# Kernel tuning notes

Hardware: AMD Instinct MI355X
Metric: run time of the kernel (lower is better)

## Reference

```python
import jax, jax.numpy as jnp
import numpy as np

N, K, B, D, H = 256, 128, 256, 256, 512  # code length, info bits, batch, embed dim, MLP hidden


def _mlp(x, W1, b1, W2, b2):
    return jnp.maximum(x @ W1 + b1, 0.0) @ W2 + b2


def setup_inputs():
    key = jax.random.key(0)
    ks = jax.random.split(key, 12)
    perm = np.random.RandomState(0).permutation(N)
    info_set = jnp.sort(jnp.asarray(perm[:K], dtype=jnp.int32))  # unique sorted info positions
    info_bits = jax.random.randint(ks[0], (B, K), 0, 2, dtype=jnp.int32)
    rv = jax.random.uniform(ks[1], (B, N), dtype=jnp.float32)  # one uniform per leaf (sampling)

    def w(k, shape, fan):
        return jax.random.normal(k, shape, jnp.float32) / np.float32(np.sqrt(fan))

    return {
        'info_bits': info_bits,
        'rv': rv,
        'info_set': info_set,
        'obs_emb': w(ks[2], (3, D), D),
        'label_emb': w(ks[3], (3, D), D),
        'cn_W1': w(ks[4], (2 * D, H), 2 * D), 'cn_b1': jnp.zeros((H,), jnp.float32),
        'cn_W2': w(ks[5], (H, D), H), 'cn_b2': jnp.zeros((D,), jnp.float32),
        'bn_W1': w(ks[6], (3 * D, H), 3 * D), 'bn_b1': jnp.zeros((H,), jnp.float32),
        'bn_W2': w(ks[7], (H, D), H), 'bn_b2': jnp.zeros((D,), jnp.float32),
        'llr_W': w(ks[8], (D, 2), D), 'llr_b': jnp.zeros((2,), jnp.float32),
    }


def reference(info_bits, rv, info_set, obs_emb, label_emb,
              cn_W1, cn_b1, cn_W2, cn_b2, bn_W1, bn_b1, bn_W2, bn_b2, llr_W, llr_b):
    batch = info_bits.shape[0]

    def encode(e, f, off, n):
        # e: (B, n, D) float embeddings; f: (B, n, 1) int32 bits (2 == unknown -> sample)
        if n == 1:
            p_uy = jax.nn.softmax(e @ llr_W + llr_b, axis=-1)        # (B, 1, 2) probs
            r = rv[:, off:off + 1]                                    # (B, 1)
            # rv > cdf[...,0] == rv > p(u=0): sample a hard bit
            hard = (r > p_uy[..., 0]).astype(jnp.int32)[..., None]    # (B, 1, 1)
            x = jnp.where(f == 2, hard, f)
            return x, x, p_uy
        half = n // 2
        e_odd, e_even = e[:, ::2], e[:, 1::2]                         # SplitEvenOdd(axis=1)
        f_left, f_right = f[:, :half], f[:, half:]
        u1est = _mlp(jnp.concatenate([e_odd, e_even], -1), cn_W1, cn_b1, cn_W2, cn_b2)
        u1, h1, p_left = encode(u1est, f_left, off, half)
        u_emb = label_emb[h1[..., 0]]                                 # (B, half, D)
        u2est = _mlp(jnp.concatenate([e_odd, e_even, u_emb], -1), bn_W1, bn_b1, bn_W2, bn_b2)
        u2, h2, p_right = encode(u2est, f_right, off + half, half)
        u = jnp.concatenate([u1, u2], 1)
        p_uy = jnp.concatenate([p_left, p_right], 1)
        v_xor = jnp.mod(h1 + h2, 2)
        # Interleave(axis=1): out[::2] = v_xor, out[1::2] = h2
        x = jnp.stack([v_xor, h2], axis=2).reshape(batch, n, 1)
        return u, x, p_uy

    # scatter info bits into the length-N frame (frozen positions stay == 2)
    u_ = jnp.full((batch, N), 2, jnp.int32).at[:, info_set].set(info_bits)
    f = u_[..., None]
    # embedding_observations_nn(2 * ones): embedding of token '2' everywhere
    e = jnp.broadcast_to(obs_emb[2], (batch, N, D))
    u, x, p_u = encode(e, f, 0, N)
    # f: sampled frame with info positions re-masked to 2
    f_out = u[..., 0].at[:, info_set].set(2)[..., None]
    return x, f_out, u, p_u
```

## Files before the change

### kernel.cpp

```cpp
#include <hip/hip_runtime.h>
#include <math.h>

#define NB 256
#define NN 256
#define NK 128
#define ND 256
#define NH 512
#define NT 1024

#define OUT_X 0
#define OUT_F 65536
#define OUT_U 131072
#define OUT_P 196608

#define EPB   65280
#define SP6O  EPB
#define S1O   (SP6O + 1024)
#define S2O   (S1O + 512)
#define S3O   (S2O + 1024)
#define LOFFI (S3O + 2048)
#define BPB   (LOFFI + 256)

__host__ __device__ __forceinline__ int loff(int d) { return 256 - (1 << (9 - d)); }

template <int PC>
__device__ void g1ks(const float* __restrict__ Abuf, float* __restrict__ part,
                     const int tid, const float* __restrict__ W1) {
  const int q = tid >> 8;
  const int c0 = (tid & 255) << 1;
  const float* Wp = W1 + (size_t)(q * 128) * NH + c0;
  const float* Ar = Abuf + q * 128;
  float a0[PC], a1[PC];
#pragma unroll
  for (int r = 0; r < PC; ++r) { a0[r] = 0.f; a1[r] = 0.f; }
  float2 n0 = *(const float2*)Wp;
  float2 n1 = *(const float2*)(Wp + NH);
  float2 n2 = *(const float2*)(Wp + 2 * NH);
  float2 n3 = *(const float2*)(Wp + 3 * NH);
#pragma unroll 2
  for (int kc = 0; kc < 124; kc += 4) {
    const float2 w0 = n0, w1 = n1, w2 = n2, w3 = n3;
    const float* Wn = Wp + (size_t)(kc + 4) * NH;
    n0 = *(const float2*)Wn;
    n1 = *(const float2*)(Wn + NH);
    n2 = *(const float2*)(Wn + 2 * NH);
    n3 = *(const float2*)(Wn + 3 * NH);
#pragma unroll
    for (int r = 0; r < PC; ++r) {
      const float4 av = *(const float4*)(Ar + r * 512 + kc);
      a0[r] += av.x * w0.x + av.y * w1.x + av.z * w2.x + av.w * w3.x;
      a1[r] += av.x * w0.y + av.y * w1.y + av.z * w2.y + av.w * w3.y;
    }
  }
#pragma unroll
  for (int r = 0; r < PC; ++r) {
    const float4 av = *(const float4*)(Ar + r * 512 + 124);
    a0[r] += av.x * n0.x + av.y * n1.x + av.z * n2.x + av.w * n3.x;
    a1[r] += av.x * n0.y + av.y * n1.y + av.z * n2.y + av.w * n3.y;
  }
#pragma unroll
  for (int r = 0; r < PC; ++r)
    *(float2*)&part[(q * PC + r) * 512 + c0] = make_float2(a0[r], a1[r]);
}

template <int RT>
__device__ void g2ks(const float* __restrict__ hid, const int hidBase,
                     float* __restrict__ part, const int tid,
                     const float* __restrict__ W2) {
  const int q = tid >> 7;
  const int c0 = (tid & 127) << 1;
  const float* Wp = W2 + (size_t)(q * 64) * ND + c0;
  const float* Hr = hid + hidBase * 512 + q * 64;
  float a0[RT], a1[RT];
#pragma unroll
  for (int r = 0; r < RT; ++r) { a0[r] = 0.f; a1[r] = 0.f; }
  float2 n0 = *(const float2*)Wp;
  float2 n1 = *(const float2*)(Wp + ND);
  float2 n2 = *(const float2*)(Wp + 2 * ND);
  float2 n3 = *(const float2*)(Wp + 3 * ND);
#pragma unroll 2
  for (int kc = 0; kc < 60; kc += 4) {
    const float2 w0 = n0, w1 = n1, w2 = n2, w3 = n3;
    const float* Wn = Wp + (size_t)(kc + 4) * ND;
    n0 = *(const float2*)Wn;
    n1 = *(const float2*)(Wn + ND);
    n2 = *(const float2*)(Wn + 2 * ND);
    n3 = *(const float2*)(Wn + 3 * ND);
#pragma unroll
    for (int r = 0; r < RT; ++r) {
      const float4 av = *(const float4*)(Hr + r * 512 + kc);
      a0[r] += av.x * w0.x + av.y * w1.x + av.z * w2.x + av.w * w3.x;
      a1[r] += av.x * w0.y + av.y * w1.y + av.z * w2.y + av.w * w3.y;
    }
  }
#pragma unroll
  for (int r = 0; r < RT; ++r) {
    const float4 av = *(const float4*)(Hr + r * 512 + 60);
    a0[r] += av.x * n0.x + av.y * n1.x + av.z * n2.x + av.w * n3.x;
    a1[r] += av.x * n0.y + av.y * n1.y + av.z * n2.y + av.w * n3.y;
  }
#pragma unroll
  for (int r = 0; r < RT; ++r)
    *(float2*)&part[(q * RT + r) * 256 + c0] = make_float2(a0[r], a1[r]);
}

template <int PC>
__device__ void g1q(const float* __restrict__ Abuf, float* __restrict__ part,
                    const int tid, const float* __restrict__ W1) {
  const int q = tid >> 7;
  const int c0 = (tid & 127) << 2;
  const float* Wp = W1 + (size_t)(q * 64) * NH + c0;
  const float* Ar = Abuf + q * 64;
  float a0[PC], a1[PC], a2[PC], a3[PC];
#pragma unroll
  for (int r = 0; r < PC; ++r) { a0[r] = 0.f; a1[r] = 0.f; a2[r] = 0.f; a3[r] = 0.f; }
  float4 n0 = *(const float4*)Wp;
  float4 n1 = *(const float4*)(Wp + NH);
  float4 n2 = *(const float4*)(Wp + 2 * NH);
  float4 n3 = *(const float4*)(Wp + 3 * NH);
#pragma unroll 2
  for (int kc = 0; kc < 60; kc += 4) {
    const float4 w0 = n0, w1 = n1, w2 = n2, w3 = n3;
    const float* Wn = Wp + (size_t)(kc + 4) * NH;
    n0 = *(const float4*)Wn;
    n1 = *(const float4*)(Wn + NH);
    n2 = *(const float4*)(Wn + 2 * NH);
    n3 = *(const float4*)(Wn + 3 * NH);
#pragma unroll
    for (int r = 0; r < PC; ++r) {
      const float4 av = *(const float4*)(Ar + r * 512 + kc);
      a0[r] += av.x * w0.x + av.y * w1.x + av.z * w2.x + av.w * w3.x;
      a1[r] += av.x * w0.y + av.y * w1.y + av.z * w2.y + av.w * w3.y;
      a2[r] += av.x * w0.z + av.y * w1.z + av.z * w2.z + av.w * w3.z;
      a3[r] += av.x * w0.w + av.y * w1.w + av.z * w2.w + av.w * w3.w;
    }
  }
#pragma unroll
  for (int r = 0; r < PC; ++r) {
    const float4 av = *(const float4*)(Ar + r * 512 + 60);
    a0[r] += av.x * n0.x + av.y * n1.x + av.z * n2.x + av.w * n3.x;
    a1[r] += av.x * n0.y + av.y * n1.y + av.z * n2.y + av.w * n3.y;
    a2[r] += av.x * n0.z + av.y * n1.z + av.z * n2.z + av.w * n3.z;
    a3[r] += av.x * n0.w + av.y * n1.w + av.z * n2.w + av.w * n3.w;
  }
#pragma unroll
  for (int r = 0; r < PC; ++r)
    *(float4*)&part[(q * PC + r) * 512 + c0] = make_float4(a0[r], a1[r], a2[r], a3[r]);
}

template <int RT>
__device__ void g2q(const float* __restrict__ hid, const int hidBase,
                    float* __restrict__ part, const int tid,
                    const float* __restrict__ W2) {
  const int q = tid >> 6;
  const int c0 = (tid & 63) << 2;
  const float* Wp = W2 + (size_t)(q * 32) * ND + c0;
  const float* Hr = hid + hidBase * 512 + q * 32;
  float a0[RT], a1[RT], a2[RT], a3[RT];
#pragma unroll
  for (int r = 0; r < RT; ++r) { a0[r] = 0.f; a1[r] = 0.f; a2[r] = 0.f; a3[r] = 0.f; }
  float4 n0 = *(const float4*)Wp;
  float4 n1 = *(const float4*)(Wp + ND);
  float4 n2 = *(const float4*)(Wp + 2 * ND);
  float4 n3 = *(const float4*)(Wp + 3 * ND);
#pragma unroll 2
  for (int kc = 0; kc < 28; kc += 4) {
    const float4 w0 = n0, w1 = n1, w2 = n2, w3 = n3;
    const float* Wn = Wp + (size_t)(kc + 4) * ND;
    n0 = *(const float4*)Wn;
    n1 = *(const float4*)(Wn + ND);
    n2 = *(const float4*)(Wn + 2 * ND);
    n3 = *(const float4*)(Wn + 3 * ND);
#pragma unroll
    for (int r = 0; r < RT; ++r) {
      const float4 av = *(const float4*)(Hr + r * 512 + kc);
      a0[r] += av.x * w0.x + av.y * w1.x + av.z * w2.x + av.w * w3.x;
      a1[r] += av.x * w0.y + av.y * w1.y + av.z * w2.y + av.w * w3.y;
      a2[r] += av.x * w0.z + av.y * w1.z + av.z * w2.z + av.w * w3.z;
      a3[r] += av.x * w0.w + av.y * w1.w + av.z * w2.w + av.w * w3.w;
    }
  }
#pragma unroll
  for (int r = 0; r < RT; ++r) {
    const float4 av = *(const float4*)(Hr + r * 512 + 28);
    a0[r] += av.x * n0.x + av.y * n1.x + av.z * n2.x + av.w * n3.x;
    a1[r] += av.x * n0.y + av.y * n1.y + av.z * n2.y + av.w * n3.y;
    a2[r] += av.x * n0.z + av.y * n1.z + av.z * n2.z + av.w * n3.z;
    a3[r] += av.x * n0.w + av.y * n1.w + av.z * n2.w + av.w * n3.w;
  }
#pragma unroll
  for (int r = 0; r < RT; ++r)
    *(float4*)&part[(q * RT + r) * 256 + c0] = make_float4(a0[r], a1[r], a2[r], a3[r]);
}

template <int KS, int PC>
__device__ void g1red(const float* __restrict__ part, float* __restrict__ hid,
                      const int tid, const float* __restrict__ b1,
                      const int isBn, const float* __restrict__ embS,
                      const int* __restrict__ bitR) {
  for (int i = tid; i < PC * 256; i += NT) {
    const int r = i >> 8, c0 = (i & 255) << 1;
    float2 s = *(const float2*)(b1 + c0);
#pragma unroll
    for (int qq = 0; qq < KS; ++qq) {
      const float2 p = *(const float2*)&part[(qq * PC + r) * 512 + c0];
      s.x += p.x; s.y += p.y;
    }
    if (isBn) {
      const float2 e = *(const float2*)&embS[bitR[r] * 512 + c0];
      s.x += e.x; s.y += e.y;
    }
    *(float2*)&hid[r * 512 + c0] = make_float2(fmaxf(s.x, 0.f), fmaxf(s.y, 0.f));
  }
}

template <int KS, int R>
__device__ void g1redspec(const float* __restrict__ part, float* __restrict__ hid,
                          const int base, const int tid,
                          const float* __restrict__ b1,
                          const float* __restrict__ embS) {
  for (int i = tid; i < R * 256; i += NT) {
    const int r = i >> 8, c0 = (i & 255) << 1;
    float2 s = *(const float2*)(b1 + c0);
#pragma unroll
    for (int qq = 0; qq < KS; ++qq) {
      const float2 p = *(const float2*)&part[(qq * R + r) * 512 + c0];
      s.x += p.x; s.y += p.y;
    }
    const float2 e0 = *(const float2*)&embS[c0];
    const float2 e1 = *(const float2*)&embS[512 + c0];
    *(float2*)&hid[(base + 2 * r) * 512 + c0] =
        make_float2(fmaxf(s.x + e0.x, 0.f), fmaxf(s.y + e0.y, 0.f));
    *(float2*)&hid[(base + 2 * r + 1) * 512 + c0] =
        make_float2(fmaxf(s.x + e1.x, 0.f), fmaxf(s.y + e1.y, 0.f));
  }
}

template <int KS, int RT>
__device__ void g2red(const float* __restrict__ part, const int tid,
                      const float* __restrict__ b2,
                      float* const* __restrict__ rowDst) {
  for (int i = tid; i < RT * 128; i += NT) {
    const int r = i >> 7, c0 = (i & 127) << 1;
    float2 s = *(const float2*)(b2 + c0);
#pragma unroll
    for (int qq = 0; qq < KS; ++qq) {
      const float2 p = *(const float2*)&part[(qq * RT + r) * 256 + c0];
      s.x += p.x; s.y += p.y;
    }
    *(float2*)(rowDst[r] + c0) = s;
  }
}

__global__ __launch_bounds__(NT, 4) void sc_quad(
    const int* __restrict__ info_bits, const float* __restrict__ rv,
    const int* __restrict__ info_set,
    const float* __restrict__ obs_emb, const float* __restrict__ label_emb,
    const float* __restrict__ cnW1, const float* __restrict__ cnb1,
    const float* __restrict__ cnW2, const float* __restrict__ cnb2,
    const float* __restrict__ bnW1, const float* __restrict__ bnb1,
    const float* __restrict__ bnW2, const float* __restrict__ bnb2,
    const float* __restrict__ llrW, const float* __restrict__ llrb,
    float* __restrict__ out, float* __restrict__ ws) {
  __shared__ float A[4096];
  __shared__ float part[20480];
  __shared__ float hid[8192];
  __shared__ float embS[1024];
  __shared__ float rowBuf[256];
  __shared__ float* rowDst[16];
  __shared__ int fmap[256];
  __shared__ int curS[256], nxtS[256];
  __shared__ float red[8];
  __shared__ int bitR[8];
  __shared__ int qbS[4];

  const int tid = threadIdx.x, b = blockIdx.x;
  float* wsb = ws + (size_t)b * BPB;
  float* E = wsb;
  float* sp6 = wsb + SP6O;
  float* S1 = wsb + S1O;
  float* S2 = wsb + S2O;
  float* S3 = wsb + S3O;
  int* Lb = (int*)(wsb + LOFFI);
  const float* obs2 = obs_emb + 2 * ND;

  {
    const int bit = tid >> 9, col = tid & 511;
    float s = 0.f;
#pragma unroll 4
    for (int j = 0; j < ND; ++j)
      s += label_emb[bit * ND + j] * bnW1[(size_t)(NH + j) * NH + col];
    embS[bit * 512 + col] = s;
  }
  if (tid < 256) fmap[tid] = -1;
  __syncthreads();
  if (tid < NK) fmap[info_set[tid]] = tid;
  __syncthreads();

  auto stageA = [&](const float* Ed, int p0, int R) {
    const int n4 = R * 128;
    float4* A4 = (float4*)A;
    if (Ed) {
      const float4* s4 = (const float4*)(Ed + (size_t)(2 * p0) * ND);
      for (int i = tid; i < n4; i += NT) A4[i] = s4[i];
    } else {
      const float4* o4 = (const float4*)obs2;
      for (int i = tid; i < n4; i += NT) A4[i] = o4[i & 63];
    }
  };

  auto plainPass = [&](int d, int isBn) {
    const int P = 1 << (7 - d);
    const float* W1 = isBn ? bnW1 : cnW1;
    const float* B1 = isBn ? bnb1 : cnb1;
    const float* W2 = isBn ? bnW2 : cnW2;
    const float* B2 = isBn ? bnb2 : cnb2;
    const float* Ed = (d == 0) ? nullptr : E + (size_t)loff(d) * ND;
    float* dstE = E + (size_t)loff(d + 1) * ND;
    const int PC = P >= 8 ? 8 : 4;
    for (int p0 = 0; p0 < P; p0 += PC) {
      stageA(Ed, p0, PC);
      if (isBn && tid < PC) bitR[tid] = Lb[loff(d + 1) + p0 + tid];
      if (tid < PC) rowDst[tid] = dstE + (size_t)(p0 + tid) * ND;
      __syncthreads();
      if (PC == 8) {
        g1ks<8>(A, part, tid, W1); __syncthreads();
        g1red<4, 8>(part, hid, tid, B1, isBn, embS, bitR); __syncthreads();
        g2ks<8>(hid, 0, part, tid, W2); __syncthreads();
        g2red<8, 8>(part, tid, B2, rowDst); __syncthreads();
      } else {
        g1q<4>(A, part, tid, W1); __syncthreads();
        g1red<8, 4>(part, hid, tid, B1, isBn, embS, bitR); __syncthreads();
        g2q<4>(hid, 0, part, tid, W2); __syncthreads();
        g2red<16, 4>(part, tid, B2, rowDst); __syncthreads();
      }
    }
  };

  auto uniPass = [&](int d) {
    const int P = 1 << (7 - d);
    const float* Ed = (d == 0) ? nullptr : E + (size_t)loff(d) * ND;
    float* dstE = E + (size_t)loff(d + 1) * ND;
    stageA(Ed, 0, 1);
    if (tid == 0) rowDst[0] = rowBuf;
    __syncthreads();
    g1q<1>(A, part, tid, cnW1); __syncthreads();
    g1red<8, 1>(part, hid, tid, cnb1, 0, embS, bitR); __syncthreads();
    g2q<1>(hid, 0, part, tid, cnW2); __syncthreads();
    g2red<16, 1>(part, tid, cnb2, rowDst); __syncthreads();
    for (int i = tid; i < P * 256; i += NT) dstE[i] = rowBuf[i & 255];
    __syncthreads();
  };

  auto pair6 = [&]() {
    stageA(E + (size_t)loff(6) * ND, 0, 2);
    if (tid < 2) rowDst[tid] = E + (size_t)(252 + tid) * ND;
    __syncthreads();
    g1q<2>(A, part, tid, cnW1); __syncthreads();
    g1red<8, 2>(part, hid, tid, cnb1, 0, embS, bitR); __syncthreads();
    g2q<2>(hid, 0, part, tid, cnW2); __syncthreads();
    g2red<16, 2>(part, tid, cnb2, rowDst); __syncthreads();
    g1q<2>(A, part, tid, bnW1); __syncthreads();
    g1redspec<8, 2>(part, hid, 2, tid, bnb1, embS); __syncthreads();
    g2q<4>(hid, 2, part, tid, bnW2);
    if (tid < 4) rowDst[tid] = sp6 + (size_t)tid * ND;
    __syncthreads();
    g2red<16, 4>(part, tid, bnb2, rowDst); __syncthreads();
  };

  auto comb = [&]() {
    for (int i = tid; i < 5 * 128; i += NT) {
      const int r = i >> 7, k = (i & 127) << 2;
      const int h = k >> 8;
      const float* src;
      if (r == 0) src = E + (size_t)(252 + h) * ND;
      else {
        const int cc = r - 1;
        const int bit = (h == 0) ? (cc >> 1) : (cc & 1);
        src = sp6 + (size_t)(h * 2 + bit) * ND;
      }
      *(float4*)&A[r * 512 + k] = *(const float4*)&src[k & 255];
    }
    __syncthreads();
    g1q<5>(A, part, tid, cnW1); __syncthreads();
    g1red<8, 5>(part, hid, tid, cnb1, 0, embS, bitR); __syncthreads();
    g2q<5>(hid, 0, part, tid, cnW2);
    if (tid < 5) rowDst[tid] = (tid == 0) ? (E + (size_t)254 * ND)
                                          : (S2 + (size_t)(tid - 1) * ND);
    __syncthreads();
    g2red<16, 5>(part, tid, cnb2, rowDst); __syncthreads();
    g1q<5>(A, part, tid, bnW1); __syncthreads();
    g1redspec<8, 5>(part, hid, 5, tid, bnb1, embS); __syncthreads();
    g2ks<10>(hid, 5, part, tid, bnW2);
    if (tid < 10) rowDst[tid] = (tid < 2) ? (S1 + (size_t)tid * ND)
                                          : (S3 + (size_t)(tid - 2) * ND);
    __syncthreads();
    g2red<8, 10>(part, tid, bnb2, rowDst); __syncthreads();
  };

  auto leaf = [&](int off) {
    const int ph = off & 3;
    const float* src;
    if (ph == 0) src = E + (size_t)254 * ND;
    else if (ph == 1) src = S1 + (size_t)qbS[0] * ND;
    else {
      const int cidx = 2 * (qbS[0] ^ qbS[1]) + qbS[1];
      src = (ph == 2) ? (S2 + (size_t)cidx * ND)
                      : (S3 + (size_t)(2 * cidx + qbS[2]) * ND);
    }
    if (tid < 256) {
      const float ev = src[tid];
      float v0 = ev * llrW[2 * tid];
      float v1 = ev * llrW[2 * tid + 1];
#pragma unroll
      for (int o = 32; o > 0; o >>= 1) {
        v0 += __shfl_down(v0, o);
        v1 += __shfl_down(v1, o);
      }
      if ((tid & 63) == 0) {
        red[tid >> 6] = v0;
        red[4 + (tid >> 6)] = v1;
      }
    }
    __syncthreads();
    if (tid == 0) {
      const float l0 = red[0] + red[1] + red[2] + red[3] + llrb[0];
      const float l1 = red[4] + red[5] + red[6] + red[7] + llrb[1];
      const float m = fmaxf(l0, l1);
      const float e0 = expf(l0 - m), e1 = expf(l1 - m);
      const float s = e0 + e1;
      const float p0 = e0 / s, p1 = e1 / s;
      const int hard = (rv[b * NN + off] > p0) ? 1 : 0;
      const int fidx = fmap[off];
      const int fval = (fidx >= 0) ? info_bits[b * NK + fidx] : 2;
      const int xb = (fval == 2) ? hard : fval;
      out[OUT_F + b * NN + off] = (fidx >= 0) ? 2.0f : (float)xb;
      out[OUT_U + b * NN + off] = (float)xb;
      out[OUT_P + (b * NN + off) * 2 + 0] = p0;
      out[OUT_P + (b * NN + off) * 2 + 1] = p1;
      curS[0] = xb;
      qbS[ph] = xb;
    }
    __syncthreads();
    int* cur = curS;
    int* nxt = nxtS;
    int len = 1, lev = 8, idx = off;
    while (idx & 1) {
      if (tid < len) {
        const int c = cur[tid];
        nxt[2 * tid] = Lb[loff(lev) + tid] ^ c;
        nxt[2 * tid + 1] = c;
      }
      __syncthreads();
      int* t = cur; cur = nxt; nxt = t;
      len <<= 1; idx >>= 1; --lev;
    }
    if (lev > 0) {
      if (tid < len) Lb[loff(lev) + tid] = cur[tid];
    } else {
      if (tid < 256) out[OUT_X + b * NN + tid] = (float)cur[tid];
    }
    __syncthreads();
  };

  for (int d = 0; d <= 5; ++d) uniPass(d);
  pair6();
  comb();

  for (int off = 0; off < NN; ++off) {
    leaf(off);
    if (off == NN - 1) break;
    const int t = off + 1;
    const int z = __ffs(t) - 1;
    if (z <= 1) continue;
    const int dbn = 7 - z;
    plainPass(dbn, 1);
    for (int d = dbn + 1; d <= 5; ++d) plainPass(d, 0);
    pair6();
    comb();
  }
}

extern "C" void kernel_launch(void* const* d_in, const int* in_sizes, int n_in,
                              void* d_out, int out_size, void* d_ws, size_t ws_size,
                              hipStream_t stream) {
  const int*   info_bits = (const int*)d_in[0];
  const float* rv        = (const float*)d_in[1];
  const int*   info_set  = (const int*)d_in[2];
  const float* obs_emb   = (const float*)d_in[3];
  const float* label_emb = (const float*)d_in[4];
  const float* cnW1      = (const float*)d_in[5];
  const float* cnb1      = (const float*)d_in[6];
  const float* cnW2      = (const float*)d_in[7];
  const float* cnb2      = (const float*)d_in[8];
  const float* bnW1      = (const float*)d_in[9];
  const float* bnb1      = (const float*)d_in[10];
  const float* bnW2      = (const float*)d_in[11];
  const float* bnb2      = (const float*)d_in[12];
  const float* llrW      = (const float*)d_in[13];
  const float* llrb      = (const float*)d_in[14];

  float* out = (float*)d_out;
  float* ws  = (float*)d_ws;

  sc_quad<<<dim3(NB), dim3(NT), 0, stream>>>(
      info_bits, rv, info_set, obs_emb, label_emb,
      cnW1, cnb1, cnW2, cnb2, bnW1, bnb1, bnW2, bnb2,
      llrW, llrb, out, ws);
}
```

Measured before the change: 10.80 ms.

## Process two batch elements per block to share MLP weight loads

Each workgroup now decodes two batch rows, stacking both rows' embeddings into the same GEMM tiles so weight reads are shared across twice as many rows. The grid is halved, and the leaf/cascade logic is duplicated per batch half within the same synchronisation steps. This trades fewer, heavier blocks (less parallelism across CUs, larger LDS footprint) for better weight reuse and fewer total barrier-bound sequential steps across the device.

Result: slower. 17.25 ms (+59.7%).

```diff
diff --git a/kernel.cpp b/kernel.cpp
--- a/kernel.cpp
+++ b/kernel.cpp
@@ -23,16 +23,16 @@
 
 __host__ __device__ __forceinline__ int loff(int d) { return 256 - (1 << (9 - d)); }
 
-template <int PC>
+template <int R>
 __device__ void g1ks(const float* __restrict__ Abuf, float* __restrict__ part,
                      const int tid, const float* __restrict__ W1) {
   const int q = tid >> 8;
   const int c0 = (tid & 255) << 1;
   const float* Wp = W1 + (size_t)(q * 128) * NH + c0;
   const float* Ar = Abuf + q * 128;
-  float a0[PC], a1[PC];
-#pragma unroll
-  for (int r = 0; r < PC; ++r) { a0[r] = 0.f; a1[r] = 0.f; }
+  float a0[R], a1[R];
+#pragma unroll
+  for (int r = 0; r < R; ++r) { a0[r] = 0.f; a1[r] = 0.f; }
   float2 n0 = *(const float2*)Wp;
   float2 n1 = *(const float2*)(Wp + NH);
   float2 n2 = *(const float2*)(Wp + 2 * NH);
@@ -46,34 +46,77 @@
     n2 = *(const float2*)(Wn + 2 * NH);
     n3 = *(const float2*)(Wn + 3 * NH);
 #pragma unroll
-    for (int r = 0; r < PC; ++r) {
+    for (int r = 0; r < R; ++r) {
       const float4 av = *(const float4*)(Ar + r * 512 + kc);
       a0[r] += av.x * w0.x + av.y * w1.x + av.z * w2.x + av.w * w3.x;
       a1[r] += av.x * w0.y + av.y * w1.y + av.z * w2.y + av.w * w3.y;
     }
   }
 #pragma unroll
-  for (int r = 0; r < PC; ++r) {
+  for (int r = 0; r < R; ++r) {
     const float4 av = *(const float4*)(Ar + r * 512 + 124);
     a0[r] += av.x * n0.x + av.y * n1.x + av.z * n2.x + av.w * n3.x;
     a1[r] += av.x * n0.y + av.y * n1.y + av.z * n2.y + av.w * n3.y;
   }
 #pragma unroll
-  for (int r = 0; r < PC; ++r)
-    *(float2*)&part[(q * PC + r) * 512 + c0] = make_float2(a0[r], a1[r]);
-}
-
-template <int RT>
-__device__ void g2ks(const float* __restrict__ hid, const int hidBase,
-                     float* __restrict__ part, const int tid,
-                     const float* __restrict__ W2) {
+  for (int r = 0; r < R; ++r)
+    *(float2*)&part[(q * R + r) * 512 + c0] = make_float2(a0[r], a1[r]);
+}
+
+template <int R>
+__device__ void g1q(const float* __restrict__ Abuf, float* __restrict__ part,
+                    const int tid, const float* __restrict__ W1) {
+  const int q = tid >> 7;
+  const int c0 = (tid & 127) << 2;
+  const float* Wp = W1 + (size_t)(q * 64) * NH + c0;
+  const float* Ar = Abuf + q * 64;
+  float a0[R], a1[R], a2[R], a3[R];
+#pragma unroll
+  for (int r = 0; r < R; ++r) { a0[r] = 0.f; a1[r] = 0.f; a2[r] = 0.f; a3[r] = 0.f; }
+  float4 n0 = *(const float4*)Wp;
+  float4 n1 = *(const float4*)(Wp + NH);
+  float4 n2 = *(const float4*)(Wp + 2 * NH);
+  float4 n3 = *(const float4*)(Wp + 3 * NH);
+#pragma unroll 2
+  for (int kc = 0; kc < 60; kc += 4) {
+    const float4 w0 = n0, w1 = n1, w2 = n2, w3 = n3;
+    const float* Wn = Wp + (size_t)(kc + 4) * NH;
+    n0 = *(const float4*)Wn;
+    n1 = *(const float4*)(Wn + NH);
+    n2 = *(const float4*)(Wn + 2 * NH);
+    n3 = *(const float4*)(Wn + 3 * NH);
+#pragma unroll
+    for (int r = 0; r < R; ++r) {
+      const float4 av = *(const float4*)(Ar + r * 512 + kc);
+      a0[r] += av.x * w0.x + av.y * w1.x + av.z * w2.x + av.w * w3.x;
+      a1[r] += av.x * w0.y + av.y * w1.y + av.z * w2.y + av.w * w3.y;
+      a2[r] += av.x * w0.z + av.y * w1.z + av.z * w2.z + av.w * w3.z;
+      a3[r] += av.x * w0.w + av.y * w1.w + av.z * w2.w + av.w * w3.w;
+    }
+  }
+#pragma unroll
+  for (int r = 0; r < R; ++r) {
+    const float4 av = *(const float4*)(Ar + r * 512 + 60);
+    a0[r] += av.x * n0.x + av.y * n1.x + av.z * n2.x + av.w * n3.x;
+    a1[r] += av.x * n0.y + av.y * n1.y + av.z * n2.y + av.w * n3.y;
+    a2[r] += av.x * n0.z + av.y * n1.z + av.z * n2.z + av.w * n3.z;
+    a3[r] += av.x * n0.w + av.y * n1.w + av.z * n2.w + av.w * n3.w;
+  }
+#pragma unroll
+  for (int r = 0; r < R; ++r)
+    *(float4*)&part[(q * R + r) * 512 + c0] = make_float4(a0[r], a1[r], a2[r], a3[r]);
+}
+
+template <int R>
+__device__ void g2ks(const float* __restrict__ Hsrc, float* __restrict__ part,
+                     const int tid, const float* __restrict__ W2) {
   const int q = tid >> 7;
   const int c0 = (tid & 127) << 1;
   const float* Wp = W2 + (size_t)(q * 64) * ND + c0;
-  const float* Hr = hid + hidBase * 512 + q * 64;
-  float a0[RT], a1[RT];
-#pragma unroll
-  for (int r = 0; r < RT; ++r) { a0[r] = 0.f; a1[r] = 0.f; }
+  const float* Hr = Hsrc + q * 64;
+  float a0[R], a1[R];
+#pragma unroll
+  for (int r = 0; r < R; ++r) { a0[r] = 0.f; a1[r] = 0.f; }
   float2 n0 = *(const float2*)Wp;
   float2 n1 = *(const float2*)(Wp + ND);
   float2 n2 = *(const float2*)(Wp + 2 * ND);
@@ -87,78 +130,33 @@
     n2 = *(const float2*)(Wn + 2 * ND);
     n3 = *(const float2*)(Wn + 3 * ND);
 #pragma unroll
-    for (int r = 0; r < RT; ++r) {
+    for (int r = 0; r < R; ++r) {
       const float4 av = *(const float4*)(Hr + r * 512 + kc);
       a0[r] += av.x * w0.x + av.y * w1.x + av.z * w2.x + av.w * w3.x;
       a1[r] += av.x * w0.y + av.y * w1.y + av.z * w2.y + av.w * w3.y;
     }
   }
 #pragma unroll
-  for (int r = 0; r < RT; ++r) {
+  for (int r = 0; r < R; ++r) {
     const float4 av = *(const float4*)(Hr + r * 512 + 60);
     a0[r] += av.x * n0.x + av.y * n1.x + av.z * n2.x + av.w * n3.x;
     a1[r] += av.x * n0.y + av.y * n1.y + av.z * n2.y + av.w * n3.y;
   }
 #pragma unroll
-  for (int r = 0; r < RT; ++r)
-    *(float2*)&part[(q * RT + r) * 256 + c0] = make_float2(a0[r], a1[r]);
-}
-
-template <int PC>
-__device__ void g1q(const float* __restrict__ Abuf, float* __restrict__ part,
-                    const int tid, const float* __restrict__ W1) {
-  const int q = tid >> 7;
-  const int c0 = (tid & 127) << 2;
-  const float* Wp = W1 + (size_t)(q * 64) * NH + c0;
-  const float* Ar = Abuf + q * 64;
-  float a0[PC], a1[PC], a2[PC], a3[PC];
-#pragma unroll
-  for (int r = 0; r < PC; ++r) { a0[r] = 0.f; a1[r] = 0.f; a2[r] = 0.f; a3[r] = 0.f; }
-  float4 n0 = *(const float4*)Wp;
-  float4 n1 = *(const float4*)(Wp + NH);
-  float4 n2 = *(const float4*)(Wp + 2 * NH);
-  float4 n3 = *(const float4*)(Wp + 3 * NH);
-#pragma unroll 2
-  for (int kc = 0; kc < 60; kc += 4) {
-    const float4 w0 = n0, w1 = n1, w2 = n2, w3 = n3;
-    const float* Wn = Wp + (size_t)(kc + 4) * NH;
-    n0 = *(const float4*)Wn;
-    n1 = *(const float4*)(Wn + NH);
-    n2 = *(const float4*)(Wn + 2 * NH);
-    n3 = *(const float4*)(Wn + 3 * NH);
-#pragma unroll
-    for (int r = 0; r < PC; ++r) {
-      const float4 av = *(const float4*)(Ar + r * 512 + kc);
-      a0[r] += av.x * w0.x + av.y * w1.x + av.z * w2.x + av.w * w3.x;
-      a1[r] += av.x * w0.y + av.y * w1.y + av.z * w2.y + av.w * w3.y;
-      a2[r] += av.x * w0.z + av.y * w1.z + av.z * w2.z + av.w * w3.z;
-      a3[r] += av.x * w0.w + av.y * w1.w + av.z * w2.w + av.w * w3.w;
-    }
-  }
-#pragma unroll
-  for (int r = 0; r < PC; ++r) {
-    const float4 av = *(const float4*)(Ar + r * 512 + 60);
-    a0[r] += av.x * n0.x + av.y * n1.x + av.z * n2.x + av.w * n3.x;
-    a1[r] += av.x * n0.y + av.y * n1.y + av.z * n2.y + av.w * n3.y;
-    a2[r] += av.x * n0.z + av.y * n1.z + av.z * n2.z + av.w * n3.z;
-    a3[r] += av.x * n0.w + av.y * n1.w + av.z * n2.w + av.w * n3.w;
-  }
-#pragma unroll
-  for (int r = 0; r < PC; ++r)
-    *(float4*)&part[(q * PC + r) * 512 + c0] = make_float4(a0[r], a1[r], a2[r], a3[r]);
-}
-
-template <int RT>
-__device__ void g2q(const float* __restrict__ hid, const int hidBase,
-                    float* __restrict__ part, const int tid,
-                    const float* __restrict__ W2) {
+  for (int r = 0; r < R; ++r)
+    *(float2*)&part[(q * R + r) * 256 + c0] = make_float2(a0[r], a1[r]);
+}
+
+template <int R>
+__device__ void g2q(const float* __restrict__ Hsrc, float* __restrict__ part,
+                    const int tid, const float* __restrict__ W2) {
   const int q = tid >> 6;
   const int c0 = (tid & 63) << 2;
   const float* Wp = W2 + (size_t)(q * 32) * ND + c0;
-  const float* Hr = hid + hidBase * 512 + q * 32;
-  float a0[RT], a1[RT], a2[RT], a3[RT];
-#pragma unroll
-  for (int r = 0; r < RT; ++r) { a0[r] = 0.f; a1[r] = 0.f; a2[r] = 0.f; a3[r] = 0.f; }
+  const float* Hr = Hsrc + q * 32;
+  float a0[R], a1[R], a2[R], a3[R];
+#pragma unroll
+  for (int r = 0; r < R; ++r) { a0[r] = 0.f; a1[r] = 0.f; a2[r] = 0.f; a3[r] = 0.f; }
   float4 n0 = *(const float4*)Wp;
   float4 n1 = *(const float4*)(Wp + ND);
   float4 n2 = *(const float4*)(Wp + 2 * ND);
@@ -172,7 +170,7 @@
     n2 = *(const float4*)(Wn + 2 * ND);
     n3 = *(const float4*)(Wn + 3 * ND);
 #pragma unroll
-    for (int r = 0; r < RT; ++r) {
+    for (int r = 0; r < R; ++r) {
       const float4 av = *(const float4*)(Hr + r * 512 + kc);
       a0[r] += av.x * w0.x + av.y * w1.x + av.z * w2.x + av.w * w3.x;
       a1[r] += av.x * w0.y + av.y * w1.y + av.z * w2.y + av.w * w3.y;
@@ -181,7 +179,7 @@
     }
   }
 #pragma unroll
-  for (int r = 0; r < RT; ++r) {
+  for (int r = 0; r < R; ++r) {
     const float4 av = *(const float4*)(Hr + r * 512 + 28);
     a0[r] += av.x * n0.x + av.y * n1.x + av.z * n2.x + av.w * n3.x;
     a1[r] += av.x * n0.y + av.y * n1.y + av.z * n2.y + av.w * n3.y;
@@ -189,21 +187,21 @@
     a3[r] += av.x * n0.w + av.y * n1.w + av.z * n2.w + av.w * n3.w;
   }
 #pragma unroll
-  for (int r = 0; r < RT; ++r)
-    *(float4*)&part[(q * RT + r) * 256 + c0] = make_float4(a0[r], a1[r], a2[r], a3[r]);
-}
-
-template <int KS, int PC>
+  for (int r = 0; r < R; ++r)
+    *(float4*)&part[(q * R + r) * 256 + c0] = make_float4(a0[r], a1[r], a2[r], a3[r]);
+}
+
+template <int KS, int R>
 __device__ void g1red(const float* __restrict__ part, float* __restrict__ hid,
                       const int tid, const float* __restrict__ b1,
                       const int isBn, const float* __restrict__ embS,
                       const int* __restrict__ bitR) {
-  for (int i = tid; i < PC * 256; i += NT) {
+  for (int i = tid; i < R * 256; i += NT) {
     const int r = i >> 8, c0 = (i & 255) << 1;
     float2 s = *(const float2*)(b1 + c0);
 #pragma unroll
     for (int qq = 0; qq < KS; ++qq) {
-      const float2 p = *(const float2*)&part[(qq * PC + r) * 512 + c0];
+      const float2 p = *(const float2*)&part[(qq * R + r) * 512 + c0];
       s.x += p.x; s.y += p.y;
     }
     if (isBn) {
@@ -215,10 +213,10 @@
 }
 
 template <int KS, int R>
-__device__ void g1redspec(const float* __restrict__ part, float* __restrict__ hid,
-                          const int base, const int tid,
-                          const float* __restrict__ b1,
-                          const float* __restrict__ embS) {
+__device__ void g1redspec2(const float* __restrict__ part, float* __restrict__ d0,
+                           float* __restrict__ d1, const int splitRow, const int tid,
+                           const float* __restrict__ b1,
+                           const float* __restrict__ embS) {
   for (int i = tid; i < R * 256; i += NT) {
     const int r = i >> 8, c0 = (i & 255) << 1;
     float2 s = *(const float2*)(b1 + c0);
@@ -229,30 +227,31 @@
     }
     const float2 e0 = *(const float2*)&embS[c0];
     const float2 e1 = *(const float2*)&embS[512 + c0];
-    *(float2*)&hid[(base + 2 * r) * 512 + c0] =
-        make_float2(fmaxf(s.x + e0.x, 0.f), fmaxf(s.y + e0.y, 0.f));
-    *(float2*)&hid[(base + 2 * r + 1) * 512 + c0] =
-        make_float2(fmaxf(s.x + e1.x, 0.f), fmaxf(s.y + e1.y, 0.f));
-  }
-}
-
-template <int KS, int RT>
+    const int o0 = 2 * r, o1 = 2 * r + 1;
+    float* w0 = (o0 < splitRow) ? (d0 + (size_t)o0 * 512) : (d1 + (size_t)(o0 - splitRow) * 512);
+    float* w1 = (o1 < splitRow) ? (d0 + (size_t)o1 * 512) : (d1 + (size_t)(o1 - splitRow) * 512);
+    *(float2*)&w0[c0] = make_float2(fmaxf(s.x + e0.x, 0.f), fmaxf(s.y + e0.y, 0.f));
+    *(float2*)&w1[c0] = make_float2(fmaxf(s.x + e1.x, 0.f), fmaxf(s.y + e1.y, 0.f));
+  }
+}
+
+template <int KS, int R>
 __device__ void g2red(const float* __restrict__ part, const int tid,
                       const float* __restrict__ b2,
                       float* const* __restrict__ rowDst) {
-  for (int i = tid; i < RT * 128; i += NT) {
+  for (int i = tid; i < R * 128; i += NT) {
     const int r = i >> 7, c0 = (i & 127) << 1;
     float2 s = *(const float2*)(b2 + c0);
 #pragma unroll
     for (int qq = 0; qq < KS; ++qq) {
-      const float2 p = *(const float2*)&part[(qq * RT + r) * 256 + c0];
+      const float2 p = *(const float2*)&part[(qq * R + r) * 256 + c0];
       s.x += p.x; s.y += p.y;
     }
     *(float2*)(rowDst[r] + c0) = s;
   }
 }
 
-__global__ __launch_bounds__(NT, 4) void sc_quad(
+__global__ __launch_bounds__(NT, 4) void sc_b2(
     const int* __restrict__ info_bits, const float* __restrict__ rv,
     const int* __restrict__ info_set,
     const float* __restrict__ obs_emb, const float* __restrict__ label_emb,
@@ -262,26 +261,27 @@
     const float* __restrict__ bnW2, const float* __restrict__ bnb2,
     const float* __restrict__ llrW, const float* __restrict__ llrb,
     float* __restrict__ out, float* __restrict__ ws) {
-  __shared__ float A[4096];
-  __shared__ float part[20480];
-  __shared__ float hid[8192];
+  __shared__ float A[5120];
+  __shared__ float partS[20480];
+  __shared__ float hid[10240];
   __shared__ float embS[1024];
   __shared__ float rowBuf[256];
   __shared__ float* rowDst[16];
   __shared__ int fmap[256];
-  __shared__ int curS[256], nxtS[256];
-  __shared__ float red[8];
+  __shared__ float red[16];
   __shared__ int bitR[8];
-  __shared__ int qbS[4];
-
-  const int tid = threadIdx.x, b = blockIdx.x;
-  float* wsb = ws + (size_t)b * BPB;
-  float* E = wsb;
-  float* sp6 = wsb + SP6O;
-  float* S1 = wsb + S1O;
-  float* S2 = wsb + S2O;
-  float* S3 = wsb + S3O;
-  int* Lb = (int*)(wsb + LOFFI);
+  __shared__ int qbS[8];
+
+  const int tid = threadIdx.x;
+  const int b0 = blockIdx.x * 2;
+  float* wsb0 = ws + (size_t)b0 * BPB;
+  float* wsb1 = ws + (size_t)(b0 + 1) * BPB;
+  float* E0 = wsb0;               float* E1 = wsb1;
+  float* sp6_0 = wsb0 + SP6O;     float* sp6_1 = wsb1 + SP6O;
+  float* S1_0 = wsb0 + S1O;       float* S1_1 = wsb1 + S1O;
+  float* S2_0 = wsb0 + S2O;       float* S2_1 = wsb1 + S2O;
+  float* S3_0 = wsb0 + S3O;       float* S3_1 = wsb1 + S3O;
+  int* Lb0 = (int*)(wsb0 + LOFFI); int* Lb1 = (int*)(wsb1 + LOFFI);
   const float* obs2 = obs_emb + 2 * ND;
 
   {
@@ -297,15 +297,19 @@
   if (tid < NK) fmap[info_set[tid]] = tid;
   __syncthreads();
 
-  auto stageA = [&](const float* Ed, int p0, int R) {
-    const int n4 = R * 128;
-    float4* A4 = (float4*)A;
-    if (Ed) {
-      const float4* s4 = (const float4*)(Ed + (size_t)(2 * p0) * ND);
-      for (int i = tid; i < n4; i += NT) A4[i] = s4[i];
-    } else {
-      const float4* o4 = (const float4*)obs2;
-      for (int i = tid; i < n4; i += NT) A4[i] = o4[i & 63];
+  auto stagePlain = [&](int d, int p0, int CH) {
+    const int n4 = 2 * CH * 128;
+    for (int i = tid; i < n4; i += NT) {
+      const int r = i >> 7, qq = i & 127, k = qq * 4;
+      float4 v;
+      if (d == 0) {
+        v = *(const float4*)&obs2[k & 255];
+      } else {
+        const float* Eu = (r < CH) ? E0 : E1;
+        const int p = p0 + ((r < CH) ? r : r - CH);
+        v = *(const float4*)&Eu[(size_t)(loff(d) + 2 * p + (k >> 8)) * ND + (k & 255)];
+      }
+      *(float4*)&A[r * 512 + k] = v;
     }
   };
 
@@ -315,150 +319,205 @@
     const float* B1 = isBn ? bnb1 : cnb1;
     const float* W2 = isBn ? bnW2 : cnW2;
     const float* B2 = isBn ? bnb2 : cnb2;
-    const float* Ed = (d == 0) ? nullptr : E + (size_t)loff(d) * ND;
-    float* dstE = E + (size_t)loff(d + 1) * ND;
-    const int PC = P >= 8 ? 8 : 4;
-    for (int p0 = 0; p0 < P; p0 += PC) {
-      stageA(Ed, p0, PC);
-      if (isBn && tid < PC) bitR[tid] = Lb[loff(d + 1) + p0 + tid];
-      if (tid < PC) rowDst[tid] = dstE + (size_t)(p0 + tid) * ND;
+    const int CH = (P >= 4) ? 4 : P;
+    for (int p0 = 0; p0 < P; p0 += CH) {
+      stagePlain(d, p0, CH);
+      if (isBn && tid < 2 * CH) {
+        const int batch = tid >= CH;
+        const int p = p0 + (batch ? tid - CH : tid);
+        bitR[tid] = (batch ? Lb1 : Lb0)[loff(d + 1) + p];
+      }
+      if (tid < 2 * CH) {
+        const int batch = tid >= CH;
+        const int p = p0 + (batch ? tid - CH : tid);
+        rowDst[tid] = (batch ? E1 : E0) + (size_t)(loff(d + 1) + p) * ND;
+      }
       __syncthreads();
-      if (PC == 8) {
-        g1ks<8>(A, part, tid, W1); __syncthreads();
-        g1red<4, 8>(part, hid, tid, B1, isBn, embS, bitR); __syncthreads();
-        g2ks<8>(hid, 0, part, tid, W2); __syncthreads();
-        g2red<8, 8>(part, tid, B2, rowDst); __syncthreads();
-      } else {
-        g1q<4>(A, part, tid, W1); __syncthreads();
-        g1red<8, 4>(part, hid, tid, B1, isBn, embS, bitR); __syncthreads();
-        g2q<4>(hid, 0, part, tid, W2); __syncthreads();
-        g2red<16, 4>(part, tid, B2, rowDst); __syncthreads();
-      }
+      g1ks<8>(A, partS, tid, W1); __syncthreads();
+      g1red<4, 8>(partS, hid, tid, B1, isBn, embS, bitR); __syncthreads();
+      g2ks<8>(hid, partS, tid, W2); __syncthreads();
+      g2red<8, 8>(partS, tid, B2, rowDst); __syncthreads();
     }
   };
 
   auto uniPass = [&](int d) {
     const int P = 1 << (7 - d);
-    const float* Ed = (d == 0) ? nullptr : E + (size_t)loff(d) * ND;
-    float* dstE = E + (size_t)loff(d + 1) * ND;
-    stageA(Ed, 0, 1);
+    for (int i = tid; i < 128; i += NT) {
+      const int k = (i & 127) * 4;
+      float4 v;
+      if (d == 0) v = *(const float4*)&obs2[k & 255];
+      else v = *(const float4*)&E0[(size_t)(loff(d) + (k >> 8)) * ND + (k & 255)];
+      *(float4*)&A[k] = v;
+    }
     if (tid == 0) rowDst[0] = rowBuf;
     __syncthreads();
-    g1q<1>(A, part, tid, cnW1); __syncthreads();
-    g1red<8, 1>(part, hid, tid, cnb1, 0, embS, bitR); __syncthreads();
-    g2q<1>(hid, 0, part, tid, cnW2); __syncthreads();
-    g2red<16, 1>(part, tid, cnb2, rowDst); __syncthreads();
-    for (int i = tid; i < P * 256; i += NT) dstE[i] = rowBuf[i & 255];
+    g1q<1>(A, partS, tid, cnW1); __syncthreads();
+    g1red<8, 1>(partS, hid, tid, cnb1, 0, embS, bitR); __syncthreads();
+    g2q<1>(hid, partS, tid, cnW2); __syncthreads();
+    g2red<16, 1>(partS, tid, cnb2, rowDst); __syncthreads();
+    float* d0 = E0 + (size_t)loff(d + 1) * ND;
+    float* d1 = E1 + (size_t)loff(d + 1) * ND;
+    for (int i = tid; i < P * 256; i += NT) {
+      const float v = rowBuf[i & 255];
+      d0[i] = v; d1[i] = v;
+    }
     __syncthreads();
   };
 
   auto pair6 = [&]() {
-    stageA(E + (size_t)loff(6) * ND, 0, 2);
-    if (tid < 2) rowDst[tid] = E + (size_t)(252 + tid) * ND;
-    __syncthreads();
-    g1q<2>(A, part, tid, cnW1); __syncthreads();
-    g1red<8, 2>(part, hid, tid, cnb1, 0, embS, bitR); __syncthreads();
-    g2q<2>(hid, 0, part, tid, cnW2); __syncthreads();
-    g2red<16, 2>(part, tid, cnb2, rowDst); __syncthreads();
-    g1q<2>(A, part, tid, bnW1); __syncthreads();
-    g1redspec<8, 2>(part, hid, 2, tid, bnb1, embS); __syncthreads();
-    g2q<4>(hid, 2, part, tid, bnW2);
-    if (tid < 4) rowDst[tid] = sp6 + (size_t)tid * ND;
-    __syncthreads();
-    g2red<16, 4>(part, tid, bnb2, rowDst); __syncthreads();
+    for (int i = tid; i < 4 * 128; i += NT) {
+      const int r = i >> 7, qq = i & 127, k = qq * 4;
+      const float* Eu = (r < 2) ? E0 : E1;
+      const int rl = r & 1;
+      *(float4*)&A[r * 512 + k] =
+          *(const float4*)&Eu[(size_t)(248 + 2 * rl + (k >> 8)) * ND + (k & 255)];
+    }
+    if (tid < 4) {
+      const int batch = tid >> 1, rl = tid & 1;
+      rowDst[tid] = (batch ? E1 : E0) + (size_t)(252 + rl) * ND;
+    }
+    __syncthreads();
+    g1q<4>(A, partS, tid, cnW1); __syncthreads();
+    g1red<8, 4>(partS, hid, tid, cnb1, 0, embS, bitR); __syncthreads();
+    g2q<4>(hid, partS, tid, cnW2); __syncthreads();
+    g2red<16, 4>(partS, tid, cnb2, rowDst); __syncthreads();
+    g1q<4>(A, partS, tid, bnW1); __syncthreads();
+    g1redspec2<8, 4>(partS, hid + 4 * 512, hid, 8, tid, bnb1, embS); __syncthreads();
+    g2ks<8>(hid + 4 * 512, partS, tid, bnW2);
+    if (tid < 8) {
+      const int batch = tid >> 2;
+      rowDst[tid] = (batch ? sp6_1 : sp6_0) + (size_t)(tid & 3) * ND;
+    }
+    __syncthreads();
+    g2red<8, 8>(partS, tid, bnb2, rowDst); __syncthreads();
   };
 
   auto comb = [&]() {
-    for (int i = tid; i < 5 * 128; i += NT) {
-      const int r = i >> 7, k = (i & 127) << 2;
+    for (int i = tid; i < 10 * 128; i += NT) {
+      const int r = i >> 7, qq = i & 127, k = qq * 4;
       const int h = k >> 8;
+      const int batch = r >= 5;
+      const int rl = batch ? r - 5 : r;
+      const float* Eu = batch ? E1 : E0;
+      const float* spu = batch ? sp6_1 : sp6_0;
       const float* src;
-      if (r == 0) src = E + (size_t)(252 + h) * ND;
+      if (rl == 0) src = Eu + (size_t)(252 + h) * ND;
       else {
-        const int cc = r - 1;
+        const int cc = rl - 1;
         const int bit = (h == 0) ? (cc >> 1) : (cc & 1);
-        src = sp6 + (size_t)(h * 2 + bit) * ND;
+        src = spu + (size_t)(h * 2 + bit) * ND;
       }
       *(float4*)&A[r * 512 + k] = *(const float4*)&src[k & 255];
     }
     __syncthreads();
-    g1q<5>(A, part, tid, cnW1); __syncthreads();
-    g1red<8, 5>(part, hid, tid, cnb1, 0, embS, bitR); __syncthreads();
-    g2q<5>(hid, 0, part, tid, cnW2);
-    if (tid < 5) rowDst[tid] = (tid == 0) ? (E + (size_t)254 * ND)
-                                          : (S2 + (size_t)(tid - 1) * ND);
-    __syncthreads();
-    g2red<16, 5>(part, tid, cnb2, rowDst); __syncthreads();
-    g1q<5>(A, part, tid, bnW1); __syncthreads();
-    g1redspec<8, 5>(part, hid, 5, tid, bnb1, embS); __syncthreads();
-    g2ks<10>(hid, 5, part, tid, bnW2);
-    if (tid < 10) rowDst[tid] = (tid < 2) ? (S1 + (size_t)tid * ND)
-                                          : (S3 + (size_t)(tid - 2) * ND);
-    __syncthreads();
-    g2red<8, 10>(part, tid, bnb2, rowDst); __syncthreads();
+    g1ks<10>(A, partS, tid, cnW1); __syncthreads();
+    g1red<4, 10>(partS, hid, tid, cnb1, 0, embS, bitR); __syncthreads();
+    g2ks<10>(hid, partS, tid, cnW2);
+    if (tid < 10) {
+      const int batch = tid >= 5;
+      const int rl = batch ? tid - 5 : tid;
+      float* Eu = batch ? E1 : E0;
+      float* S2u = batch ? S2_1 : S2_0;
+      rowDst[tid] = (rl == 0) ? (Eu + (size_t)254 * ND) : (S2u + (size_t)(rl - 1) * ND);
+    }
+    __syncthreads();
+    g2red<8, 10>(partS, tid, cnb2, rowDst); __syncthreads();
+    g1ks<10>(A, partS, tid, bnW1); __syncthreads();
+    g1redspec2<4, 10>(partS, hid + 10 * 512, A, 10, tid, bnb1, embS); __syncthreads();
+    g2ks<10>(hid + 10 * 512, partS, tid, bnW2);
+    if (tid < 10) rowDst[tid] = (tid < 2) ? (S1_0 + (size_t)tid * ND)
+                                          : (S3_0 + (size_t)(tid - 2) * ND);
+    __syncthreads();
+    g2red<8, 10>(partS, tid, bnb2, rowDst); __syncthreads();
+    g2ks<10>(A, partS, tid, bnW2);
+    if (tid < 10) rowDst[tid] = (tid < 2) ? (S1_1 + (size_t)tid * ND)
+                                          : (S3_1 + (size_t)(tid - 2) * ND);
+    __syncthreads();
+    g2red<8, 10>(partS, tid, bnb2, rowDst); __syncthreads();
   };
 
   auto leaf = [&](int off) {
     const int ph = off & 3;
-    const float* src;
-    if (ph == 0) src = E + (size_t)254 * ND;
-    else if (ph == 1) src = S1 + (size_t)qbS[0] * ND;
-    else {
-      const int cidx = 2 * (qbS[0] ^ qbS[1]) + qbS[1];
-      src = (ph == 2) ? (S2 + (size_t)cidx * ND)
-                      : (S3 + (size_t)(2 * cidx + qbS[2]) * ND);
-    }
-    if (tid < 256) {
-      const float ev = src[tid];
-      float v0 = ev * llrW[2 * tid];
-      float v1 = ev * llrW[2 * tid + 1];
+    if (tid < 512) {
+      const int batch = tid >> 8, t = tid & 255;
+      const float* Eu = batch ? E1 : E0;
+      const float* S1u = batch ? S1_1 : S1_0;
+      const float* S2u = batch ? S2_1 : S2_0;
+      const float* S3u = batch ? S3_1 : S3_0;
+      const int* qb = qbS + batch * 4;
+      const float* src;
+      if (ph == 0) src = Eu + (size_t)254 * ND;
+      else if (ph == 1) src = S1u + (size_t)qb[0] * ND;
+      else {
+        const int cidx = 2 * (qb[0] ^ qb[1]) + qb[1];
+        src = (ph == 2) ? (S2u + (size_t)cidx * ND)
+                        : (S3u + (size_t)(2 * cidx + qb[2]) * ND);
+      }
+      const float ev = src[t];
+      float v0 = ev * llrW[2 * t];
+      float v1 = ev * llrW[2 * t + 1];
 #pragma unroll
       for (int o = 32; o > 0; o >>= 1) {
         v0 += __shfl_down(v0, o);
         v1 += __shfl_down(v1, o);
       }
-      if ((tid & 63) == 0) {
-        red[tid >> 6] = v0;
-        red[4 + (tid >> 6)] = v1;
-      }
-    }
-    __syncthreads();
-    if (tid == 0) {
-      const float l0 = red[0] + red[1] + red[2] + red[3] + llrb[0];
-      const float l1 = red[4] + red[5] + red[6] + red[7] + llrb[1];
+      const int w = tid >> 6;
+      if ((tid & 63) == 0) { red[w] = v0; red[8 + w] = v1; }
+    }
+    __syncthreads();
+    int* casc = (int*)partS;
+    int* cur0 = casc;        int* nxt0 = casc + 256;
+    int* cur1 = casc + 512;  int* nxt1 = casc + 768;
+    if (tid < 512 && (tid & 255) == 0) {
+      const int batch = tid >> 8;
+      const int bg = b0 + batch;
+      const float l0 = red[batch * 4 + 0] + red[batch * 4 + 1] +
+                       red[batch * 4 + 2] + red[batch * 4 + 3] + llrb[0];
+      const float l1 = red[8 + batch * 4 + 0] + red[8 + batch * 4 + 1] +
+                       red[8 + batch * 4 + 2] + red[8 + batch * 4 + 3] + llrb[1];
       const float m = fmaxf(l0, l1);
       const float e0 = expf(l0 - m), e1 = expf(l1 - m);
       const float s = e0 + e1;
       const float p0 = e0 / s, p1 = e1 / s;
-      const int hard = (rv[b * NN + off] > p0) ? 1 : 0;
+      const int hard = (rv[bg * NN + off] > p0) ? 1 : 0;
       const int fidx = fmap[off];
-      const int fval = (fidx >= 0) ? info_bits[b * NK + fidx] : 2;
+      const int fval = (fidx >= 0) ? info_bits[bg * NK + fidx] : 2;
       const int xb = (fval == 2) ? hard : fval;
-      out[OUT_F + b * NN + off] = (fidx >= 0) ? 2.0f : (float)xb;
-      out[OUT_U + b * NN + off] = (float)xb;
-      out[OUT_P + (b * NN + off) * 2 + 0] = p0;
-      out[OUT_P + (b * NN + off) * 2 + 1] = p1;
-      curS[0] = xb;
-      qbS[ph] = xb;
-    }
-    __syncthreads();
-    int* cur = curS;
-    int* nxt = nxtS;
+      out[OUT_F + bg * NN + off] = (fidx >= 0) ? 2.0f : (float)xb;
+      out[OUT_U + bg * NN + off] = (float)xb;
+      out[OUT_P + (bg * NN + off) * 2 + 0] = p0;
+      out[OUT_P + (bg * NN + off) * 2 + 1] = p1;
+      (batch ? cur1 : cur0)[0] = xb;
+      qbS[batch * 4 + ph] = xb;
+    }
+    __syncthreads();
     int len = 1, lev = 8, idx = off;
     while (idx & 1) {
-      if (tid < len) {
-        const int c = cur[tid];
-        nxt[2 * tid] = Lb[loff(lev) + tid] ^ c;
-        nxt[2 * tid + 1] = c;
+      if (tid < 512) {
+        const int batch = tid >> 8, t = tid & 255;
+        int* cur = batch ? cur1 : cur0;
+        int* nxt = batch ? nxt1 : nxt0;
+        const int* Lbp = batch ? Lb1 : Lb0;
+        if (t < len) {
+          const int c = cur[t];
+          nxt[2 * t] = Lbp[loff(lev) + t] ^ c;
+          nxt[2 * t + 1] = c;
+        }
       }
       __syncthreads();
-      int* t = cur; cur = nxt; nxt = t;
+      { int* t0 = cur0; cur0 = nxt0; nxt0 = t0; }
+      { int* t1 = cur1; cur1 = nxt1; nxt1 = t1; }
       len <<= 1; idx >>= 1; --lev;
     }
-    if (lev > 0) {
-      if (tid < len) Lb[loff(lev) + tid] = cur[tid];
-    } else {
-      if (tid < 256) out[OUT_X + b * NN + tid] = (float)cur[tid];
+    if (tid < 512) {
+      const int batch = tid >> 8, t = tid & 255;
+      int* cur = batch ? cur1 : cur0;
+      int* Lbp = batch ? Lb1 : Lb0;
+      if (lev > 0) {
+        if (t < len) Lbp[loff(lev) + t] = cur[t];
+      } else {
+        out[OUT_X + (size_t)(b0 + batch) * NN + t] = (float)cur[t];
+      }
     }
     __syncthreads();
   };
@@ -503,7 +562,7 @@
   float* out = (float*)d_out;
   float* ws  = (float*)d_ws;
 
-  sc_quad<<<dim3(NB), dim3(NT), 0, stream>>>(
+  sc_b2<<<dim3(NB / 2), dim3(NT), 0, stream>>>(
       info_bits, rv, info_set, obs_emb, label_emb,
       cnW1, cnb1, cnW2, cnb2, bnW1, bnb1, bnW2, bnb2,
       llrW, llrb, out, ws);
```
